# Performance work log

Hardware: AMD Instinct MI355X
Metric: run time of the kernel (lower is better)

## Reference

```python
import jax, jax.numpy as jnp
import numpy as np

N, C, T, V, S = 64, 64, 300, 25, 3
INTER = C // 4  # coff_embedding = 4
KER_T = 9      # temporal attention kernel
KER_V = V      # V=25 is odd -> spatial attention kernel = V, pad = (V-1)//2


def setup_inputs() -> dict:
    key = jax.random.key(0)
    ks = jax.random.split(key, 20)
    f = lambda k, s, scale=0.05: jax.random.normal(k, s, jnp.float32) * scale
    return {
        "x": jax.random.normal(ks[0], (N, C, T, V), jnp.float32),
        "A": f(ks[1], (S, V, V), 0.2),
        "alpha": jnp.array(0.1, jnp.float32),
        "Wa": f(ks[2], (S, INTER, C)), "ba": f(ks[3], (S, INTER)),
        "Wb": f(ks[4], (S, INTER, C)), "bb": f(ks[5], (S, INTER)),
        "Wd": f(ks[6], (S, C, C)),     "bd": f(ks[7], (S, C)),
        "bn_gamma": jnp.ones((C,), jnp.float32),
        "bn_beta": jnp.zeros((C,), jnp.float32),
        "bn_mean": f(ks[8], (C,)),
        "bn_var": jax.random.uniform(ks[9], (C,), jnp.float32) + 0.5,
        "Wsa": f(ks[10], (1, C, KER_V)), "bsa": f(ks[11], (1,)),
        "Wta": f(ks[12], (1, C, KER_T)), "bta": f(ks[13], (1,)),
        "Wfc1": f(ks[14], (C // 2, C)),  "bfc1": f(ks[15], (C // 2,)),
        "Wfc2": f(ks[16], (C, C // 2)),  "bfc2": f(ks[17], (C,)),
    }


def _conv1d(z, w, bias, pad):
    # z: [N, Cin, L], w: [Cout, Cin, K] -> [N, Cout, L]
    o = jax.lax.conv_general_dilated(z, w, (1,), [(pad, pad)],
                                     dimension_numbers=('NCH', 'OIH', 'NCH'))
    return o + bias[None, :, None]


def reference(x, A, alpha, Wa, ba, Wb, bb, Wd, bd,
              bn_gamma, bn_beta, bn_mean, bn_var,
              Wsa, bsa, Wta, bta, Wfc1, bfc1, Wfc2, bfc2):
    n, c, t, v = x.shape
    inter = Wa.shape[1]
    # adaptive adjacency per subset (1x1 convs = channel einsums)
    a = jnp.einsum('nctv,sic->nsitv', x, Wa) + ba[None, :, :, None, None]   # [N,S,inter,T,V]
    b = jnp.einsum('nctv,sic->nsitv', x, Wb) + bb[None, :, :, None, None]
    M = jnp.tanh(jnp.einsum('nsitv,nsitw->nsvw', a, b) / (inter * t))       # [N,S,V,V]
    G = A[None] + alpha * M
    # graph conv: x @ G per subset, then 1x1 conv_d, summed over subsets
    zp = jnp.einsum('nctv,nsvw->nsctw', x, G)                                # [N,S,C,T,V]
    y = jnp.einsum('nsctv,soc->notv', zp, Wd) + bd.sum(0)[None, :, None, None]
    # BN (eval) + residual (down = identity since in_c == out_c) + ReLU
    inv = bn_gamma / jnp.sqrt(bn_var + 1e-5)
    y = (y - bn_mean[None, :, None, None]) * inv[None, :, None, None] + bn_beta[None, :, None, None]
    y = jax.nn.relu(y + x)
    # spatial attention over joints
    se1 = jax.nn.sigmoid(_conv1d(y.mean(2), Wsa, bsa, (KER_V - 1) // 2))    # [N,1,V]
    y = y * se1[:, :, None, :] + y
    # temporal attention over frames
    se1 = jax.nn.sigmoid(_conv1d(y.mean(3), Wta, bta, (KER_T - 1) // 2))    # [N,1,T]
    y = y * se1[:, :, :, None] + y
    # channel attention (squeeze-excite)
    se = y.mean((2, 3))                                                      # [N,C]
    se2 = jax.nn.sigmoid(jax.nn.relu(se @ Wfc1.T + bfc1) @ Wfc2.T + bfc2)
    y = y * se2[:, :, None, None] + y
    return y
```

## Files before the change

kernel.cpp:

```cpp
#include <hip/hip_runtime.h>

typedef __bf16 bf16;
typedef bf16 bf16x8 __attribute__((ext_vector_type(8)));
typedef bf16 bf16x4 __attribute__((ext_vector_type(4)));
typedef float f32x4 __attribute__((ext_vector_type(4)));

#define WS_XG    0u
#define WS_WAB   61505536u
#define WS_WD    61517824u
#define WS_COEFA 61542400u
#define WS_COEFB 61542656u
#define WS_GT    61542912u
#define WS_MPART 61936128u
#define WS_STP   61936128u
#define WS_SE1   74519040u
#define WS_SE2   74527232u
#define WS_SE3   74605056u

__device__ __forceinline__ f32x4 mfma16(bf16x8 a, bf16x8 b, f32x4 c) {
  return __builtin_amdgcn_mfma_f32_16x16x32_bf16(a, b, c, 0, 0, 0);
}

__global__ __launch_bounds__(256) void k_prep(
    const float* __restrict__ Wa, const float* __restrict__ Wb,
    const float* __restrict__ Wd, const float* __restrict__ bd,
    const float* __restrict__ gam, const float* __restrict__ bet,
    const float* __restrict__ mean, const float* __restrict__ var,
    char* __restrict__ ws) {
  bf16* wab = (bf16*)(ws + WS_WAB);
  bf16* wd  = (bf16*)(ws + WS_WD);
  float* cA = (float*)(ws + WS_COEFA);
  float* cB = (float*)(ws + WS_COEFB);
  int tid = threadIdx.x;
  for (int f = tid; f < 3*32*64; f += 256) {
    int s = f >> 11, r = (f >> 6) & 31, c = f & 63;
    float v = (r < 16) ? Wa[(s*16 + r)*64 + c] : Wb[(s*16 + (r-16))*64 + c];
    wab[f] = (bf16)v;
  }
  for (int f = tid; f < 3*64*64; f += 256) wd[f] = (bf16)Wd[f];
  if (tid < 64) {
    float bds = bd[tid] + bd[64+tid] + bd[128+tid];
    float iv = gam[tid] / sqrtf(var[tid] + 1e-5f);
    cA[tid] = iv;
    cB[tid] = (bds - mean[tid]) * iv + bet[tid];
  }
}

__global__ __launch_bounds__(256) void k_tr(
    const float* __restrict__ x, char* __restrict__ ws) {
  __shared__ __attribute__((aligned(16))) bf16 tile[64*410];
  const int tc = blockIdx.x, n = blockIdx.y, tid = threadIdx.x;
  const int t0 = tc*16;
  const int vmax = min(400, 7500 - t0*25);
  bf16* XG = (bf16*)(ws + WS_XG);
  for (int u = tid; u < 6400; u += 256) {
    int c = u / 100, q = u % 100;
    int idx = 4*q;
    if (idx < vmax) {
      float4 val = *(const float4*)(x + (size_t)(n*64 + c)*7500 + t0*25 + idx);
      bf16* p = &tile[c*410 + idx];
      p[0] = (bf16)val.x; p[1] = (bf16)val.y; p[2] = (bf16)val.z; p[3] = (bf16)val.w;
    }
  }
  __syncthreads();
  for (int k = 0; k < 16; ++k) {
    int u = tid + k*256;
    int c8 = u & 7, v = (u >> 3) & 31, dt = u >> 8;
    int t = t0 + dt;
    if (v < 25 && t < 300) {
      bf16x8 pk;
      #pragma unroll
      for (int j = 0; j < 8; ++j) pk[j] = tile[(c8*8 + j)*410 + dt*25 + v];
      *(bf16x8*)&XG[((size_t)(n*300 + t)*25 + v)*64 + c8*8] = pk;
    }
  }
}

__global__ __launch_bounds__(256) void k1_m(
    const float* __restrict__ ba_g, const float* __restrict__ bb_g,
    char* __restrict__ ws) {
  __shared__ __attribute__((aligned(16))) bf16 AB[6*32*72];
  const int seg = blockIdx.x, n = blockIdx.y;
  const int tid = threadIdx.x;
  const int lane = tid & 63, wv = tid >> 6;
  const int l15 = lane & 15, l4 = lane >> 4;
  const int t0 = seg*19, tlen = min(19, 300 - t0);
  const bf16* XG  = (const bf16*)(ws + WS_XG);
  const bf16* wab = (const bf16*)(ws + WS_WAB);
  const f32x4 z4 = {0.f,0.f,0.f,0.f};

  bf16x8 Afr[6][2];
  float bias[6][4];
  #pragma unroll
  for (int rt = 0; rt < 6; ++rt) {
    const int s = rt >> 1, abk = rt & 1;
    #pragma unroll
    for (int kk = 0; kk < 2; ++kk)
      Afr[rt][kk] = *(const bf16x8*)&wab[(s*32 + abk*16 + l15)*64 + kk*32 + 8*l4];
    const float* bp = abk ? bb_g : ba_g;
    #pragma unroll
    for (int r = 0; r < 4; ++r) bias[rt][r] = bp[s*16 + 4*l4 + r];
  }
  f32x4 macc[3]; macc[0]=z4; macc[1]=z4; macc[2]=z4;
  const int vt2 = wv >> 1, wt2 = wv & 1;
  const int nch = (tlen + 3) >> 2;

  for (int ch = 0; ch < nch; ++ch) {
    const int tl = ch*4 + wv;
    const int t = t0 + tl;
    const bool tv = (tl < tlen);
    #pragma unroll
    for (int vt = 0; vt < 2; ++vt) {
      f32x4 acc[6];
      #pragma unroll
      for (int rt = 0; rt < 6; ++rt) acc[rt] = z4;
      #pragma unroll
      for (int kk = 0; kk < 2; ++kk) {
        bf16x8 B = *(const bf16x8*)&XG[((size_t)(n*300 + t)*25 + vt*16 + l15)*64 + kk*32 + 8*l4];
        #pragma unroll
        for (int rt = 0; rt < 6; ++rt) acc[rt] = mfma16(Afr[rt][kk], B, acc[rt]);
      }
      #pragma unroll
      for (int rt = 0; rt < 6; ++rt) {
        bf16x4 pk;
        #pragma unroll
        for (int r = 0; r < 4; ++r)
          pk[r] = (bf16)(tv ? (acc[rt][r] + bias[rt][r]) : 0.f);
        *(bf16x4*)&AB[(rt*32 + vt*16 + l15)*72 + wv*16 + 4*l4] = pk;
      }
    }
    __syncthreads();
    #pragma unroll
    for (int s = 0; s < 3; ++s) {
      #pragma unroll
      for (int kk = 0; kk < 2; ++kk) {
        bf16x8 Aa = *(const bf16x8*)&AB[((s*2 + 0)*32 + vt2*16 + l15)*72 + kk*32 + 8*l4];
        bf16x8 Bb = *(const bf16x8*)&AB[((s*2 + 1)*32 + wt2*16 + l15)*72 + kk*32 + 8*l4];
        macc[s] = mfma16(Aa, Bb, macc[s]);
      }
    }
    __syncthreads();
  }
  float* mp = (float*)(ws + WS_MPART);
  #pragma unroll
  for (int s = 0; s < 3; ++s) {
    #pragma unroll
    for (int r = 0; r < 4; ++r) {
      int v = vt2*16 + 4*l4 + r, w = wt2*16 + l15;
      mp[(((n*16 + seg)*3 + s)*32 + v)*32 + w] = macc[s][r];
    }
  }
}

__global__ __launch_bounds__(256) void k1b_g(
    const float* __restrict__ A, const float* __restrict__ alp,
    char* __restrict__ ws) {
  int e = blockIdx.x*256 + threadIdx.x;
  int w = e & 31, v = (e >> 5) & 31;
  int s = (e >> 10) % 3, n = e / 3072;
  const float* mp = (const float*)(ws + WS_MPART);
  float m = 0.f;
  #pragma unroll
  for (int p = 0; p < 16; ++p)
    m += mp[(((n*16 + p)*3 + s)*32 + v)*32 + w];
  float g = 0.f;
  if (v < 25 && w < 25)
    g = A[(s*25 + v)*25 + w] + alp[0] * tanhf(m * (1.f/4800.f));
  bf16* gt = (bf16*)(ws + WS_GT);
  gt[((n*3 + s)*32 + w)*32 + v] = (bf16)g;
}

__global__ __launch_bounds__(256, 4) void k3_y(char* __restrict__ ws) {
  __shared__ __attribute__((aligned(16))) bf16 wdL[3*64*72];
  __shared__ __attribute__((aligned(16))) bf16 ULs[4*16*96];
  const int seg = blockIdx.x, n = blockIdx.y;
  const int tid = threadIdx.x, lane = tid & 63, wv = tid >> 6;
  const int l15 = lane & 15, l4 = lane >> 4;
  const int t0 = seg*19, tlen = min(19, 300 - t0);
  const bf16* XG = (const bf16*)(ws + WS_XG);
  bf16* YG = (bf16*)(ws + WS_XG);
  const bf16* wd = (const bf16*)(ws + WS_WD);
  const bf16* gt = (const bf16*)(ws + WS_GT);
  const float* cA = (const float*)(ws + WS_COEFA);
  const float* cB = (const float*)(ws + WS_COEFB);
  const f32x4 z4 = {0.f,0.f,0.f,0.f};
  bf16* UL = &ULs[wv*16*96];

  for (int f = tid; f < 1536; f += 256) {
    int row = f >> 3, c8 = f & 7;
    *(bf16x8*)&wdL[row*72 + c8*8] = *(const bf16x8*)&wd[row*64 + c8*8];
  }
  bf16x8 Gfr[2][3];
  #pragma unroll
  for (int wt = 0; wt < 2; ++wt)
    #pragma unroll
    for (int s = 0; s < 3; ++s)
      Gfr[wt][s] = *(const bf16x8*)&gt[((n*3 + s)*32 + wt*16 + l15)*32 + 8*l4];
  __syncthreads();

  const int tb = (tlen*wv) >> 2, te = (tlen*(wv+1)) >> 2;
  float st[4][2][4] = {};

  for (int tl = tb; tl < te; ++tl) {
    const size_t rowb = (size_t)(n*300 + t0 + tl)*25;
    bf16x8 Bv[2][2];
    #pragma unroll
    for (int vt = 0; vt < 2; ++vt)
      #pragma unroll
      for (int kk = 0; kk < 2; ++kk)
        Bv[vt][kk] = *(const bf16x8*)&XG[(rowb + vt*16 + l15)*64 + kk*32 + 8*l4];
    #pragma unroll
    for (int ot = 0; ot < 4; ++ot) {
      #pragma unroll
      for (int s = 0; s < 3; ++s) {
        bf16x8 W0 = *(const bf16x8*)&wdL[(s*64 + ot*16 + l15)*72 + 8*l4];
        bf16x8 W1 = *(const bf16x8*)&wdL[(s*64 + ot*16 + l15)*72 + 32 + 8*l4];
        #pragma unroll
        for (int vt = 0; vt < 2; ++vt) {
          f32x4 acc = mfma16(W0, Bv[vt][0], z4);
          acc = mfma16(W1, Bv[vt][1], acc);
          #pragma unroll
          for (int r = 0; r < 4; ++r)
            UL[(4*l4 + r)*96 + s*32 + vt*16 + l15] = (bf16)acc[r];
        }
      }
      f32x4 acc2[2] = {z4, z4};
      #pragma unroll
      for (int s = 0; s < 3; ++s) {
        bf16x8 Aa = *(const bf16x8*)&UL[l15*96 + s*32 + 8*l4];
        acc2[0] = mfma16(Aa, Gfr[0][s], acc2[0]);
        acc2[1] = mfma16(Aa, Gfr[1][s], acc2[1]);
      }
      const int o0 = ot*16 + 4*l4;
      const f32x4 cAr = *(const f32x4*)&cA[o0];
      const f32x4 cBr = *(const f32x4*)&cB[o0];
      #pragma unroll
      for (int wt = 0; wt < 2; ++wt) {
        const int w = wt*16 + l15;
        bf16x4 Rx = *(const bf16x4*)&XG[(rowb + w)*64 + o0];
        if (w < 25) {
          bf16x4 pk;
          #pragma unroll
          for (int r = 0; r < 4; ++r) {
            float val = fmaxf(acc2[wt][r]*cAr[r] + cBr[r] + (float)Rx[r], 0.f);
            pk[r] = (bf16)val;
            st[ot][wt][r] += val;
          }
          *(bf16x4*)&YG[(rowb + w)*64 + o0] = pk;
        }
      }
    }
  }
  float* LDSf = (float*)wdL;
  float* stp = (float*)(ws + WS_STP);
  #pragma unroll
  for (int half = 0; half < 2; ++half) {
    __syncthreads();
    #pragma unroll
    for (int ot2 = 0; ot2 < 2; ++ot2)
      #pragma unroll
      for (int wt = 0; wt < 2; ++wt)
        #pragma unroll
        for (int r = 0; r < 4; ++r)
          LDSf[wv*1056 + (ot2*16 + 4*l4 + r)*33 + wt*16 + l15] = st[half*2 + ot2][wt][r];
    __syncthreads();
    for (int e = tid; e < 800; e += 256) {
      int o = e / 25, w = e % 25;
      float sum = LDSf[o*33 + w] + LDSf[1056 + o*33 + w]
                + LDSf[2112 + o*33 + w] + LDSf[3168 + o*33 + w];
      stp[((n*16 + seg)*64 + half*32 + o)*25 + w] = sum;
    }
  }
}

__global__ __launch_bounds__(1024) void k_att(
    const float* __restrict__ Wsa, const float* __restrict__ bsa,
    const float* __restrict__ Wta, const float* __restrict__ bta,
    const float* __restrict__ Wfc1, const float* __restrict__ bfc1,
    const float* __restrict__ Wfc2, const float* __restrict__ bfc2,
    char* __restrict__ ws) {
  __shared__ float Sm[64][26];
  __shared__ float red0[25][8];
  __shared__ float w1[25];
  __shared__ bf16 Sv[64][304];
  __shared__ float WLa[576];
  __shared__ float redt[304][4];
  __shared__ float w2s[304];
  __shared__ float red2[64][16];
  __shared__ float mS[64];
  __shared__ float hS[32];
  const int n = blockIdx.x, tid = threadIdx.x;
  const float* stp = (const float*)(ws + WS_STP);
  const bf16* YG = (const bf16*)(ws + WS_XG);

  for (int f = tid; f < 1600; f += 1024) {
    int c = f / 25, v = f % 25;
    float s = 0.f;
    #pragma unroll
    for (int p = 0; p < 16; ++p) s += stp[((n*16 + p)*64 + c)*25 + v];
    Sm[c][v] = s * (1.f/300.f);
  }
  for (int f = tid; f < 576; f += 1024) WLa[f] = Wta[f];
  __syncthreads();
  if (tid < 200) {
    int v = tid >> 3, part = tid & 7;
    float acc = 0.f;
    for (int c = part; c < 64; c += 8) {
      #pragma unroll
      for (int k = 0; k < 25; ++k) {
        int vv = v + k - 12;
        if (vv >= 0 && vv < 25) acc += Wsa[c*25 + k] * Sm[c][vv];
      }
    }
    red0[v][part] = acc;
  }
  __syncthreads();
  if (tid < 25) {
    float a = bsa[0];
    #pragma unroll
    for (int p = 0; p < 8; ++p) a += red0[tid][p];
    float f1 = 1.f + 1.f/(1.f + expf(-a));
    w1[tid] = f1;
    ((float*)(ws + WS_SE1))[n*32 + tid] = f1;
  }
  __syncthreads();
  {
    const int wvid = tid >> 6, lane = tid & 63;
    for (int iter = 0; iter < 19; ++iter) {
      int t = iter*16 + wvid;
      if (t < 300) {
        float acc = 0.f;
        #pragma unroll
        for (int v = 0; v < 25; ++v)
          acc += w1[v] * (float)YG[(((size_t)n*300 + t)*25 + v)*64 + lane];
        Sv[lane][t] = (bf16)acc;
      }
    }
  }
  __syncthreads();
  for (int u = tid; u < 1200; u += 1024) {
    int t = u >> 2, part = u & 3;
    float acc = 0.f;
    for (int c = part*16; c < part*16 + 16; ++c) {
      #pragma unroll
      for (int k = 0; k < 9; ++k) {
        int t2 = t + k - 4;
        if (t2 >= 0 && t2 < 300) acc += WLa[c*9 + k] * (float)Sv[c][t2];
      }
    }
    redt[t][part] = acc;
  }
  __syncthreads();
  if (tid < 300) {
    float a = (redt[tid][0] + redt[tid][1] + redt[tid][2] + redt[tid][3]) * (1.f/25.f) + bta[0];
    float f2 = 1.f + 1.f/(1.f + expf(-a));
    w2s[tid] = f2;
    ((float*)(ws + WS_SE2))[n*304 + tid] = f2;
  }
  __syncthreads();
  {
    int c = tid & 63, part = tid >> 6;
    int tb = part*19, te = min(tb + 19, 300);
    float acc = 0.f;
    for (int t = tb; t < te; ++t) acc += w2s[t] * (float)Sv[c][t];
    red2[c][part] = acc;
  }
  __syncthreads();
  if (tid < 64) {
    float mm = 0.f;
    #pragma unroll
    for (int p = 0; p < 16; ++p) mm += red2[tid][p];
    mS[tid] = mm * (1.f/7500.f);
  }
  __syncthreads();
  if (tid < 32) {
    float a = bfc1[tid];
    for (int c = 0; c < 64; ++c) a += Wfc1[tid*64 + c] * mS[c];
    hS[tid] = fmaxf(a, 0.f);
  }
  __syncthreads();
  if (tid < 64) {
    float a = bfc2[tid];
    #pragma unroll
    for (int j = 0; j < 32; ++j) a += Wfc2[tid*32 + j] * hS[j];
    ((float*)(ws + WS_SE3))[n*64 + tid] = 1.f + 1.f/(1.f + expf(-a));
  }
}

__global__ __launch_bounds__(256) void k7_scale(
    const char* __restrict__ ws, float* __restrict__ out) {
  __shared__ float tile[200][66];
  __shared__ float w3S[64];
  const int tc = blockIdx.x, n = blockIdx.y, tid = threadIdx.x;
  const bf16* YG = (const bf16*)(ws + WS_XG);
  const float* w1 = (const float*)(ws + WS_SE1) + n*32;
  const float* w2 = (const float*)(ws + WS_SE2) + n*304;
  if (tid < 64) w3S[tid] = ((const float*)(ws + WS_SE3))[n*64 + tid];
  __syncthreads();
  #pragma unroll
  for (int sub = 0; sub < 2; ++sub) {
    const int tb = tc*16 + sub*8;
    const int nT = min(8, 300 - tb);
    if (nT <= 0) break;
    const int rowlen = nT*25;
    for (int u = tid; u < rowlen*8; u += 256) {
      int c8 = u & 7, rest = u >> 3;
      int v = rest % 25, dt = rest / 25;
      int t = tb + dt;
      bf16x8 val = *(const bf16x8*)&YG[(((size_t)n*300 + t)*25 + v)*64 + c8*8];
      float sc = w1[v] * w2[t];
      float* dst = &tile[dt*25 + v][c8*8];
      #pragma unroll
      for (int j = 0; j < 8; ++j) dst[j] = (float)val[j] * sc * w3S[c8*8 + j];
    }
    __syncthreads();
    for (int u = tid; u < 64*rowlen; u += 256) {
      int c = u / rowlen, q = u % rowlen;
      out[(size_t)(n*64 + c)*7500 + tb*25 + q] = tile[q][c];
    }
    __syncthreads();
  }
}

extern "C" void kernel_launch(void* const* d_in, const int* in_sizes, int n_in,
                              void* d_out, int out_size, void* d_ws, size_t ws_size,
                              hipStream_t stream) {
  const float* x    = (const float*)d_in[0];
  const float* A    = (const float*)d_in[1];
  const float* alp  = (const float*)d_in[2];
  const float* Wa   = (const float*)d_in[3];
  const float* ba   = (const float*)d_in[4];
  const float* Wb   = (const float*)d_in[5];
  const float* bb   = (const float*)d_in[6];
  const float* Wd   = (const float*)d_in[7];
  const float* bd   = (const float*)d_in[8];
  const float* gam  = (const float*)d_in[9];
  const float* bet  = (const float*)d_in[10];
  const float* mean = (const float*)d_in[11];
  const float* var  = (const float*)d_in[12];
  const float* Wsa  = (const float*)d_in[13];
  const float* bsa  = (const float*)d_in[14];
  const float* Wta  = (const float*)d_in[15];
  const float* bta  = (const float*)d_in[16];
  const float* Wfc1 = (const float*)d_in[17];
  const float* bfc1 = (const float*)d_in[18];
  const float* Wfc2 = (const float*)d_in[19];
  const float* bfc2 = (const float*)d_in[20];
  char* ws = (char*)d_ws;
  float* out = (float*)d_out;

  k_prep<<<dim3(1), dim3(256), 0, stream>>>(Wa, Wb, Wd, bd, gam, bet, mean, var, ws);
  k_tr<<<dim3(19, 64), dim3(256), 0, stream>>>(x, ws);
  k1_m<<<dim3(16, 64), dim3(256), 0, stream>>>(ba, bb, ws);
  k1b_g<<<dim3(768), dim3(256), 0, stream>>>(A, alp, ws);
  k3_y<<<dim3(16, 64), dim3(256), 0, stream>>>(ws);
  k_att<<<dim3(64), dim3(1024), 0, stream>>>(Wsa, bsa, Wta, bta, Wfc1, bfc1, Wfc2, bfc2, ws);
  k7_scale<<<dim3(19, 64), dim3(256), 0, stream>>>(ws, out);
}
```

Before: 257.3 us.

## Split attention kernel into parallel stages and halve transpose/scale tile sizes

The single 64-block attention kernel is split into three kernels: a spatial-attention kernel, a 256-block kernel that computes the joint-weighted temporal sums from the main activation buffer, and a reduced attention kernel that reads those sums from workspace. This spreads the heaviest memory read across far more workgroups than the previous one-block-per-sample kernel. The transpose and final scale kernels now use 8-frame tiles with twice as many blocks, vectorised bf16x4 LDS stores and float2 output stores. The cost is two extra kernel launches and an extra workspace round trip for the temporal sums.

```diff
diff --git a/kernel.cpp b/kernel.cpp
--- a/kernel.cpp
+++ b/kernel.cpp
@@ -13,6 +13,7 @@
 #define WS_GT    61542912u
 #define WS_MPART 61936128u
 #define WS_STP   61936128u
+#define WS_SVP   68489728u
 #define WS_SE1   74519040u
 #define WS_SE2   74527232u
 #define WS_SE3   74605056u
@@ -48,30 +49,37 @@
 
 __global__ __launch_bounds__(256) void k_tr(
     const float* __restrict__ x, char* __restrict__ ws) {
-  __shared__ __attribute__((aligned(16))) bf16 tile[64*410];
+  __shared__ __attribute__((aligned(16))) bf16 tile[64*204];
   const int tc = blockIdx.x, n = blockIdx.y, tid = threadIdx.x;
-  const int t0 = tc*16;
-  const int vmax = min(400, 7500 - t0*25);
+  const int t0 = tc*8;
+  const int vmax = min(200, 7500 - t0*25);
   bf16* XG = (bf16*)(ws + WS_XG);
-  for (int u = tid; u < 6400; u += 256) {
-    int c = u / 100, q = u % 100;
-    int idx = 4*q;
-    if (idx < vmax) {
-      float4 val = *(const float4*)(x + (size_t)(n*64 + c)*7500 + t0*25 + idx);
-      bf16* p = &tile[c*410 + idx];
-      p[0] = (bf16)val.x; p[1] = (bf16)val.y; p[2] = (bf16)val.z; p[3] = (bf16)val.w;
-    }
-  }
-  __syncthreads();
-  for (int k = 0; k < 16; ++k) {
-    int u = tid + k*256;
-    int c8 = u & 7, v = (u >> 3) & 31, dt = u >> 8;
-    int t = t0 + dt;
-    if (v < 25 && t < 300) {
-      bf16x8 pk;
-      #pragma unroll
-      for (int j = 0; j < 8; ++j) pk[j] = tile[(c8*8 + j)*410 + dt*25 + v];
-      *(bf16x8*)&XG[((size_t)(n*300 + t)*25 + v)*64 + c8*8] = pk;
+  #pragma unroll
+  for (int it = 0; it < 13; ++it) {
+    int u = it*256 + tid;
+    if (u < 3200) {
+      int c = u / 50, q = u % 50;
+      int idx = 4*q;
+      if (idx < vmax) {
+        float4 val = *(const float4*)(x + (size_t)(n*64 + c)*7500 + t0*25 + idx);
+        bf16x4 pk = {(bf16)val.x, (bf16)val.y, (bf16)val.z, (bf16)val.w};
+        *(bf16x4*)&tile[c*204 + idx] = pk;
+      }
+    }
+  }
+  __syncthreads();
+  #pragma unroll
+  for (int it = 0; it < 7; ++it) {
+    int u = it*256 + tid;
+    if (u < 1600) {
+      int c8 = u & 7, tv = u >> 3;
+      int t = t0 + tv/25, v = tv % 25;
+      if (t < 300) {
+        bf16x8 pk;
+        #pragma unroll
+        for (int j = 0; j < 8; ++j) pk[j] = tile[(c8*8 + j)*204 + tv];
+        *(bf16x8*)&XG[((size_t)(n*300 + t)*25 + v)*64 + c8*8] = pk;
+      }
     }
   }
 }
@@ -273,15 +281,66 @@
   }
 }
 
-__global__ __launch_bounds__(1024) void k_att(
+__global__ __launch_bounds__(256) void k4_se1(
     const float* __restrict__ Wsa, const float* __restrict__ bsa,
+    char* __restrict__ ws) {
+  __shared__ float Sm[64][26];
+  __shared__ float red[25][8];
+  int n = blockIdx.x, tid = threadIdx.x;
+  const float* stp = (const float*)(ws + WS_STP);
+  for (int f = tid; f < 1600; f += 256) {
+    int c = f / 25, v = f % 25;
+    float s = 0.f;
+    #pragma unroll
+    for (int p = 0; p < 16; ++p) s += stp[((n*16 + p)*64 + c)*25 + v];
+    Sm[c][v] = s * (1.f/300.f);
+  }
+  __syncthreads();
+  float acc = 0.f;
+  int v = tid >> 3, part = tid & 7;
+  if (tid < 200) {
+    for (int c = part; c < 64; c += 8) {
+      #pragma unroll
+      for (int k = 0; k < 25; ++k) {
+        int vv = v + k - 12;
+        if (vv >= 0 && vv < 25) acc += Wsa[c*25 + k] * Sm[c][vv];
+      }
+    }
+    red[v][part] = acc;
+  }
+  __syncthreads();
+  if (tid < 25) {
+    float a = bsa[0];
+    #pragma unroll
+    for (int p = 0; p < 8; ++p) a += red[tid][p];
+    ((float*)(ws + WS_SE1))[n*32 + tid] = 1.f + 1.f/(1.f + expf(-a));
+  }
+}
+
+__global__ __launch_bounds__(256) void k5_sv(char* __restrict__ ws) {
+  __shared__ float w1[25];
+  const int tq = blockIdx.x, n = blockIdx.y;
+  const int wv = threadIdx.x >> 6, lane = threadIdx.x & 63;
+  const bf16* YG = (const bf16*)(ws + WS_XG);
+  bf16* svp = (bf16*)(ws + WS_SVP);
+  if (threadIdx.x < 25) w1[threadIdx.x] = ((const float*)(ws + WS_SE1))[n*32 + threadIdx.x];
+  __syncthreads();
+  const int tb = tq*75;
+  for (int i = wv; i < 75; i += 4) {
+    const int t = tb + i;
+    float acc = 0.f;
+    #pragma unroll
+    for (int v = 0; v < 25; ++v)
+      acc += w1[v] * (float)YG[(((size_t)n*300 + t)*25 + v)*64 + lane];
+    svp[((size_t)n*304 + t)*64 + lane] = (bf16)acc;
+  }
+}
+
+__global__ __launch_bounds__(1024) void k_att2(
     const float* __restrict__ Wta, const float* __restrict__ bta,
     const float* __restrict__ Wfc1, const float* __restrict__ bfc1,
     const float* __restrict__ Wfc2, const float* __restrict__ bfc2,
     char* __restrict__ ws) {
-  __shared__ float Sm[64][26];
-  __shared__ float red0[25][8];
-  __shared__ float w1[25];
   __shared__ bf16 Sv[64][304];
   __shared__ float WLa[576];
   __shared__ float redt[304][4];
@@ -290,53 +349,13 @@
   __shared__ float mS[64];
   __shared__ float hS[32];
   const int n = blockIdx.x, tid = threadIdx.x;
-  const float* stp = (const float*)(ws + WS_STP);
-  const bf16* YG = (const bf16*)(ws + WS_XG);
-
-  for (int f = tid; f < 1600; f += 1024) {
-    int c = f / 25, v = f % 25;
-    float s = 0.f;
-    #pragma unroll
-    for (int p = 0; p < 16; ++p) s += stp[((n*16 + p)*64 + c)*25 + v];
-    Sm[c][v] = s * (1.f/300.f);
+  const bf16* svp = (const bf16*)(ws + WS_SVP);
+
+  for (int u = tid; u < 300*64; u += 1024) {
+    int t = u >> 6, c = u & 63;
+    Sv[c][t] = svp[((size_t)n*304 + t)*64 + c];
   }
   for (int f = tid; f < 576; f += 1024) WLa[f] = Wta[f];
-  __syncthreads();
-  if (tid < 200) {
-    int v = tid >> 3, part = tid & 7;
-    float acc = 0.f;
-    for (int c = part; c < 64; c += 8) {
-      #pragma unroll
-      for (int k = 0; k < 25; ++k) {
-        int vv = v + k - 12;
-        if (vv >= 0 && vv < 25) acc += Wsa[c*25 + k] * Sm[c][vv];
-      }
-    }
-    red0[v][part] = acc;
-  }
-  __syncthreads();
-  if (tid < 25) {
-    float a = bsa[0];
-    #pragma unroll
-    for (int p = 0; p < 8; ++p) a += red0[tid][p];
-    float f1 = 1.f + 1.f/(1.f + expf(-a));
-    w1[tid] = f1;
-    ((float*)(ws + WS_SE1))[n*32 + tid] = f1;
-  }
-  __syncthreads();
-  {
-    const int wvid = tid >> 6, lane = tid & 63;
-    for (int iter = 0; iter < 19; ++iter) {
-      int t = iter*16 + wvid;
-      if (t < 300) {
-        float acc = 0.f;
-        #pragma unroll
-        for (int v = 0; v < 25; ++v)
-          acc += w1[v] * (float)YG[(((size_t)n*300 + t)*25 + v)*64 + lane];
-        Sv[lane][t] = (bf16)acc;
-      }
-    }
-  }
   __syncthreads();
   for (int u = tid; u < 1200; u += 1024) {
     int t = u >> 2, part = u & 3;
@@ -389,36 +408,35 @@
 
 __global__ __launch_bounds__(256) void k7_scale(
     const char* __restrict__ ws, float* __restrict__ out) {
-  __shared__ float tile[200][66];
+  __shared__ float tile[200*65];
   __shared__ float w3S[64];
   const int tc = blockIdx.x, n = blockIdx.y, tid = threadIdx.x;
   const bf16* YG = (const bf16*)(ws + WS_XG);
   const float* w1 = (const float*)(ws + WS_SE1) + n*32;
   const float* w2 = (const float*)(ws + WS_SE2) + n*304;
   if (tid < 64) w3S[tid] = ((const float*)(ws + WS_SE3))[n*64 + tid];
-  __syncthreads();
-  #pragma unroll
-  for (int sub = 0; sub < 2; ++sub) {
-    const int tb = tc*16 + sub*8;
-    const int nT = min(8, 300 - tb);
-    if (nT <= 0) break;
-    const int rowlen = nT*25;
-    for (int u = tid; u < rowlen*8; u += 256) {
-      int c8 = u & 7, rest = u >> 3;
-      int v = rest % 25, dt = rest / 25;
-      int t = tb + dt;
-      bf16x8 val = *(const bf16x8*)&YG[(((size_t)n*300 + t)*25 + v)*64 + c8*8];
-      float sc = w1[v] * w2[t];
-      float* dst = &tile[dt*25 + v][c8*8];
-      #pragma unroll
-      for (int j = 0; j < 8; ++j) dst[j] = (float)val[j] * sc * w3S[c8*8 + j];
-    }
-    __syncthreads();
-    for (int u = tid; u < 64*rowlen; u += 256) {
-      int c = u / rowlen, q = u % rowlen;
-      out[(size_t)(n*64 + c)*7500 + tb*25 + q] = tile[q][c];
-    }
-    __syncthreads();
+  const int tb = tc*8;
+  const int nT = min(8, 300 - tb);
+  const int rowlen = nT*25;
+  __syncthreads();
+  for (int u = tid; u < rowlen*8; u += 256) {
+    int c8 = u & 7, rest = u >> 3;
+    int v = rest % 25, dt = rest / 25;
+    int t = tb + dt;
+    bf16x8 val = *(const bf16x8*)&YG[(((size_t)n*300 + t)*25 + v)*64 + c8*8];
+    float sc = w1[v] * w2[t];
+    #pragma unroll
+    for (int j = 0; j < 8; ++j)
+      tile[(dt*25 + v)*65 + c8*8 + j] = (float)val[j] * sc * w3S[c8*8 + j];
+  }
+  __syncthreads();
+  const int nq2 = rowlen >> 1;
+  for (int u = tid; u < 64*nq2; u += 256) {
+    int c = u / nq2, q2 = u % nq2;
+    float2 o;
+    o.x = tile[(2*q2)*65 + c];
+    o.y = tile[(2*q2 + 1)*65 + c];
+    *(float2*)&out[(size_t)(n*64 + c)*7500 + tb*25 + 2*q2] = o;
   }
 }
 
@@ -450,10 +468,12 @@
   float* out = (float*)d_out;
 
   k_prep<<<dim3(1), dim3(256), 0, stream>>>(Wa, Wb, Wd, bd, gam, bet, mean, var, ws);
-  k_tr<<<dim3(19, 64), dim3(256), 0, stream>>>(x, ws);
+  k_tr<<<dim3(38, 64), dim3(256), 0, stream>>>(x, ws);
   k1_m<<<dim3(16, 64), dim3(256), 0, stream>>>(ba, bb, ws);
   k1b_g<<<dim3(768), dim3(256), 0, stream>>>(A, alp, ws);
   k3_y<<<dim3(16, 64), dim3(256), 0, stream>>>(ws);
-  k_att<<<dim3(64), dim3(1024), 0, stream>>>(Wsa, bsa, Wta, bta, Wfc1, bfc1, Wfc2, bfc2, ws);
-  k7_scale<<<dim3(19, 64), dim3(256), 0, stream>>>(ws, out);
-}
+  k4_se1<<<dim3(64), dim3(256), 0, stream>>>(Wsa, bsa, ws);
+  k5_sv<<<dim3(4, 64), dim3(256), 0, stream>>>(ws);
+  k_att2<<<dim3(64), dim3(1024), 0, stream>>>(Wta, bta, Wfc1, bfc1, Wfc2, bfc2, ws);
+  k7_scale<<<dim3(38, 64), dim3(256), 0, stream>>>(ws, out);
+}
```

After: 248.4 us. -3.4%, faster.
